# Kernel optimization log

Measured on AMD Instinct MI355X. Metric: run time of the kernel, lower is better.

Reference implementation:

```python
import jax, jax.numpy as jnp
import numpy as np

B, LP, NC, D, E = 8, 1000, 64, 128, 320  # batch, protein len, compound atoms, hid dim, esm dim


def _linear_params(key, din, dout):
    k1, k2 = jax.random.split(key)
    lim = 1.0 / np.sqrt(din)
    W = jax.random.uniform(k1, (din, dout), minval=-lim, maxval=lim, dtype=jnp.float32)
    b = jax.random.uniform(k2, (dout,), minval=-lim, maxval=lim, dtype=jnp.float32)
    return W, b


def setup_inputs() -> dict:
    key = jax.random.key(0)
    ks = jax.random.split(key, 14)
    inp = {
        "protein_embedding": jax.random.normal(ks[0], (B, LP, E), dtype=jnp.float32),
        "protein_feat_x": jax.random.normal(ks[1], (B, LP, D), dtype=jnp.float32),
        "compound_feats": jax.random.normal(ks[2], (B, NC, D), dtype=jnp.float32),
    }
    layers = [("emb", E, D), ("wq", D, D), ("wk", D, D), ("wv", D, D), ("wo", D, D),
              ("jp", D, D), ("jc", D, D),
              ("c1", D, 1024), ("c2", 1024, 1024), ("c3", 1024, 256), ("c4", 256, 1)]
    for i, (name, din, dout) in enumerate(layers):
        W, b = _linear_params(ks[3 + i], din, dout)
        inp[name + "_w"] = W
        inp[name + "_b"] = b
    return inp


def reference(protein_embedding, protein_feat_x, compound_feats,
              emb_w, emb_b, wq_w, wq_b, wk_w, wk_b, wv_w, wv_b, wo_w, wo_b,
              jp_w, jp_b, jc_w, jc_b,
              c1_w, c1_b, c2_w, c2_b, c3_w, c3_b, c4_w, c4_b):
    # protein sequence embedding -> hid dim
    pe = protein_embedding @ emb_w + emb_b                      # [B, LP, D]
    # single-head cross attention: query = seq embedding, key/value = graph feats
    Q = pe @ wq_w + wq_b
    K = protein_feat_x @ wk_w + wk_b
    V = protein_feat_x @ wv_w + wv_b
    scale = jnp.sqrt(jnp.asarray(D, pe.dtype))                  # n_heads=1 -> head_dim=D
    attn = jax.nn.softmax(jnp.einsum('bqd,bkd->bqk', Q, K) / scale, axis=-1)
    protein_feats = jnp.einsum('bqk,bkd->bqd', attn, V) @ wo_w + wo_b  # [B, LP, D]

    # sigmoid bilinear joint attention over (protein residue, compound atom) pairs
    P = jax.nn.relu(protein_feats) @ jp_w + jp_b                # [B, LP, D]
    C = jax.nn.relu(compound_feats) @ jc_w + jc_b               # [B, NC, D]
    A = jax.nn.sigmoid(jnp.einsum('bid,bkd->bik', P, C))        # [B, LP, NC]
    A = A / jnp.sum(A, axis=(1, 2), keepdims=True)

    # tanh outer product (the costly 4D bikj intermediate) then weighted reduction
    cp = jnp.tanh(protein_feats[:, :, None, :] * compound_feats[:, None, :, :])  # [B, LP, NC, D]
    cp_embedding = jnp.einsum('bikd,bik->bd', cp, A)            # [B, D]

    # classifier MLP (dropout is eval-mode identity)
    h = jax.nn.relu(cp_embedding @ c1_w + c1_b)
    h = jax.nn.relu(h @ c2_w + c2_b)
    h = jax.nn.relu(h @ c3_w + c3_b)
    return h @ c4_w + c4_b                                      # [B, 1]
```

## Files before the change

kernel.cpp:

```cpp
#include <hip/hip_runtime.h>
#include <hip/hip_bf16.h>
#include <math.h>

#define LP 1000
#define NCMP 64
#define NSPLIT 3

__device__ __forceinline__ float rcp_fast(float x) { return __builtin_amdgcn_rcpf(x); }

template<bool RELU_IN>
__device__ __forceinline__ void gemm_body(const float* X, const float* W, const float* __restrict__ bias,
                                          float* Y, int K, int rowbase)
{
    __shared__ __align__(16) float Ws[32][128];
    __shared__ __align__(16) float Xt[32][36];
    const int t  = threadIdx.x;
    const int r0 = (t >> 5) * 4;
    const int c0 = (t & 31) * 4;
    const int xr = t >> 3, xk = (t & 7) << 2;
    const int xrow = rowbase + xr;
    float4 xv = *(const float4*)(X + (long)xrow * K + xk);
    float4 wv[4];
    #pragma unroll
    for (int u = 0; u < 4; ++u) {
        int s = t + u * 256, r = s >> 5, cb = (s & 31) << 2;
        wv[u] = *(const float4*)(W + (long)r * 128 + cb);
    }
    float acc[4][4] = {};
    for (int k0 = 0; k0 < K; k0 += 32) {
        float4 xs = xv;
        if (RELU_IN) { xs.x = fmaxf(xs.x,0.f); xs.y = fmaxf(xs.y,0.f);
                       xs.z = fmaxf(xs.z,0.f); xs.w = fmaxf(xs.w,0.f); }
        Xt[xk+0][xr] = xs.x; Xt[xk+1][xr] = xs.y; Xt[xk+2][xr] = xs.z; Xt[xk+3][xr] = xs.w;
        #pragma unroll
        for (int u = 0; u < 4; ++u) {
            int s = t + u * 256, r = s >> 5, cb = (s & 31) << 2;
            *(float4*)&Ws[r][cb] = wv[u];
        }
        __syncthreads();
        if (k0 + 32 < K) {
            xv = *(const float4*)(X + (long)xrow * K + k0 + 32 + xk);
            #pragma unroll
            for (int u = 0; u < 4; ++u) {
                int s = t + u * 256, r = s >> 5, cb = (s & 31) << 2;
                wv[u] = *(const float4*)(W + (long)(k0 + 32 + r) * 128 + cb);
            }
        }
        #pragma unroll
        for (int kk = 0; kk < 32; ++kk) {
            float4 w4 = *(const float4*)&Ws[kk][c0];
            float4 x4 = *(const float4*)&Xt[kk][r0];
            acc[0][0] = fmaf(x4.x, w4.x, acc[0][0]); acc[0][1] = fmaf(x4.x, w4.y, acc[0][1]);
            acc[0][2] = fmaf(x4.x, w4.z, acc[0][2]); acc[0][3] = fmaf(x4.x, w4.w, acc[0][3]);
            acc[1][0] = fmaf(x4.y, w4.x, acc[1][0]); acc[1][1] = fmaf(x4.y, w4.y, acc[1][1]);
            acc[1][2] = fmaf(x4.y, w4.z, acc[1][2]); acc[1][3] = fmaf(x4.y, w4.w, acc[1][3]);
            acc[2][0] = fmaf(x4.z, w4.x, acc[2][0]); acc[2][1] = fmaf(x4.z, w4.y, acc[2][1]);
            acc[2][2] = fmaf(x4.z, w4.z, acc[2][2]); acc[2][3] = fmaf(x4.z, w4.w, acc[2][3]);
            acc[3][0] = fmaf(x4.w, w4.x, acc[3][0]); acc[3][1] = fmaf(x4.w, w4.y, acc[3][1]);
            acc[3][2] = fmaf(x4.w, w4.z, acc[3][2]); acc[3][3] = fmaf(x4.w, w4.w, acc[3][3]);
        }
        __syncthreads();
    }
    float4 bv = *(const float4*)(bias + c0);
    #pragma unroll
    for (int i = 0; i < 4; ++i) {
        int row = rowbase + r0 + i;
        float4 o;
        o.x = acc[i][0] + bv.x; o.y = acc[i][1] + bv.y;
        o.z = acc[i][2] + bv.z; o.w = acc[i][3] + bv.w;
        *(float4*)(Y + (long)row * 128 + c0) = o;
    }
}

__global__ __launch_bounds__(256) void pre0_k(const float* __restrict__ emb_w, const float* __restrict__ emb_b,
                                              const float* __restrict__ wq_w, const float* __restrict__ wq_b,
                                              const float* __restrict__ wv_w, const float* __restrict__ wv_b,
                                              const float* __restrict__ wo_w, const float* __restrict__ wo_b,
                                              const float* __restrict__ zeros,
                                              float* __restrict__ Wp, float* __restrict__ bp,
                                              float* __restrict__ Wvo, float* __restrict__ bvo)
{
    const int bid = blockIdx.x;
    if (bid < 10) { gemm_body<false>(emb_w, wq_w, zeros, Wp, 128, bid * 32); return; }
    if (bid >= 11 && bid < 15) { gemm_body<false>(wv_w, wo_w, zeros, Wvo, 128, (bid - 11) * 32); return; }
    int n = threadIdx.x;
    if (n < 128) {
        const float* vb = (bid == 10) ? emb_b : wv_b;
        const float* Wm = (bid == 10) ? wq_w  : wo_w;
        const float* ab = (bid == 10) ? wq_b  : wo_b;
        float a0 = 0.f, a1 = 0.f, a2 = 0.f, a3 = 0.f;
        for (int k = 0; k < 128; k += 4) {
            a0 = fmaf(vb[k+0], Wm[(k+0)*128 + n], a0);
            a1 = fmaf(vb[k+1], Wm[(k+1)*128 + n], a1);
            a2 = fmaf(vb[k+2], Wm[(k+2)*128 + n], a2);
            a3 = fmaf(vb[k+3], Wm[(k+3)*128 + n], a3);
        }
        float* dst = (bid == 10) ? bp : bvo;
        dst[n] = (a0 + a1) + (a2 + a3) + ab[n];
    }
}

__global__ __launch_bounds__(256) void qkv_k(const float* __restrict__ PE, const float* __restrict__ Wp,
                                             const float* __restrict__ bp, const float* __restrict__ PFX,
                                             const float* __restrict__ wk_w, const float* __restrict__ wk_b,
                                             const float* __restrict__ CF, const float* __restrict__ jc_w,
                                             const float* __restrict__ jc_b,
                                             float* __restrict__ Qo, float* __restrict__ Ko, float* __restrict__ Cj)
{
    if (blockIdx.x < 250)
        gemm_body<false>(PE, Wp, bp, Qo, 320, blockIdx.x * 32);
    else if (blockIdx.x < 500)
        gemm_body<false>(PFX, wk_w, wk_b, Ko, 128, (blockIdx.x - 250) * 32);
    else
        gemm_body<true>(CF, jc_w, jc_b, Cj, 128, (blockIdx.x - 500) * 32);
}

__global__ __launch_bounds__(256) void flash6_k(const float* __restrict__ Q, const float* __restrict__ Kg,
                                                const float* __restrict__ Vg, float* __restrict__ Opart,
                                                float* __restrict__ mpart, float* __restrict__ lpart)
{
    __shared__ __align__(16) float Qs[48][132];
    __shared__ __align__(16) float KVs[64][132];
    __shared__ __align__(16) float Ps[48][68];
    const int t  = threadIdx.x;
    const int tr = t >> 4;
    const int tc = t & 15;
    const int qt = blockIdx.x, sp = blockIdx.y, b = blockIdx.z;
    const int q0 = qt * 48;
    const int kt0 = (sp * 16) / NSPLIT;
    const int kt1 = ((sp + 1) * 16) / NSPLIT;
    const float SCALE = 0.08838834764831845f;
    const float L2E   = 1.4426950408889634f;

    #pragma unroll
    for (int u = 0; u < 6; ++u) {
        int s = t + u * 256, r = s >> 5, cb = (s & 31) << 2;
        float4 v = make_float4(0.f, 0.f, 0.f, 0.f);
        if (q0 + r < LP) v = *(const float4*)(Q + ((long)b * LP + q0 + r) * 128 + cb);
        *(float4*)&Qs[r][cb] = v;
    }
    float m_i[3] = { -3.0e38f, -3.0e38f, -3.0e38f };
    float l_i[3] = { 0.f, 0.f, 0.f };
    float Oa[3][8] = {};

    for (int kt = kt0; kt < kt1; ++kt) {
        const int key0 = kt * 64;
        __syncthreads();
        #pragma unroll
        for (int u = 0; u < 8; ++u) {
            int s = t + u * 256, r = s >> 5, cb = (s & 31) << 2;
            float4 v = make_float4(0.f, 0.f, 0.f, 0.f);
            if (key0 + r < LP) v = *(const float4*)(Kg + ((long)b * LP + key0 + r) * 128 + cb);
            *(float4*)&KVs[r][cb] = v;
        }
        __syncthreads();
        float sacc[3][4] = {};
        #pragma unroll 4
        for (int d4 = 0; d4 < 32; ++d4) {
            float4 q0v = *(const float4*)&Qs[3 * tr + 0][d4 << 2];
            float4 q1v = *(const float4*)&Qs[3 * tr + 1][d4 << 2];
            float4 q2v = *(const float4*)&Qs[3 * tr + 2][d4 << 2];
            #pragma unroll
            for (int j = 0; j < 4; ++j) {
                float4 kv = *(const float4*)&KVs[tc + (j << 4)][d4 << 2];
                sacc[0][j] += q0v.x*kv.x + q0v.y*kv.y + q0v.z*kv.z + q0v.w*kv.w;
                sacc[1][j] += q1v.x*kv.x + q1v.y*kv.y + q1v.z*kv.z + q1v.w*kv.w;
                sacc[2][j] += q2v.x*kv.x + q2v.y*kv.y + q2v.z*kv.z + q2v.w*kv.w;
            }
        }
        __syncthreads();
        float4 vreg[8];
        #pragma unroll
        for (int u = 0; u < 8; ++u) {
            int s = t + u * 256, r = s >> 5, cb = (s & 31) << 2;
            vreg[u] = make_float4(0.f, 0.f, 0.f, 0.f);
            if (key0 + r < LP) vreg[u] = *(const float4*)(Vg + ((long)b * LP + key0 + r) * 128 + cb);
        }
        #pragma unroll
        for (int j = 0; j < 4; ++j) {
            bool valid = (key0 + tc + (j << 4)) < LP;
            #pragma unroll
            for (int i = 0; i < 3; ++i) {
                float sv = sacc[i][j] * SCALE;
                sacc[i][j] = valid ? sv : -3.0e38f;
            }
        }
        #pragma unroll
        for (int i = 0; i < 3; ++i) {
            float tm = fmaxf(fmaxf(sacc[i][0], sacc[i][1]), fmaxf(sacc[i][2], sacc[i][3]));
            tm = fmaxf(tm, __shfl_xor(tm, 1));
            tm = fmaxf(tm, __shfl_xor(tm, 2));
            tm = fmaxf(tm, __shfl_xor(tm, 4));
            tm = fmaxf(tm, __shfl_xor(tm, 8));
            float mnew  = fmaxf(m_i[i], tm);
            float alpha = exp2f((m_i[i] - mnew) * L2E);
            float ps = 0.f;
            #pragma unroll
            for (int j = 0; j < 4; ++j) {
                float p = exp2f((sacc[i][j] - mnew) * L2E);
                Ps[3 * tr + i][tc + (j << 4)] = p;
                ps += p;
            }
            ps += __shfl_xor(ps, 1);
            ps += __shfl_xor(ps, 2);
            ps += __shfl_xor(ps, 4);
            ps += __shfl_xor(ps, 8);
            l_i[i] = l_i[i] * alpha + ps;
            m_i[i] = mnew;
            #pragma unroll
            for (int j = 0; j < 8; ++j) Oa[i][j] *= alpha;
        }
        #pragma unroll
        for (int u = 0; u < 8; ++u) {
            int s = t + u * 256, r = s >> 5, cb = (s & 31) << 2;
            *(float4*)&KVs[r][cb] = vreg[u];
        }
        __syncthreads();
        #pragma unroll 2
        for (int cg = 0; cg < 16; ++cg) {
            float4 pa = *(const float4*)&Ps[3 * tr + 0][cg << 2];
            float4 pb = *(const float4*)&Ps[3 * tr + 1][cg << 2];
            float4 pc = *(const float4*)&Ps[3 * tr + 2][cg << 2];
            #pragma unroll
            for (int e = 0; e < 4; ++e) {
                int c = (cg << 2) + e;
                float4 va = *(const float4*)&KVs[c][tc << 2];
                float4 vb = *(const float4*)&KVs[c][64 + (tc << 2)];
                float p0 = (e == 0) ? pa.x : (e == 1) ? pa.y : (e == 2) ? pa.z : pa.w;
                float p1 = (e == 0) ? pb.x : (e == 1) ? pb.y : (e == 2) ? pb.z : pb.w;
                float p2 = (e == 0) ? pc.x : (e == 1) ? pc.y : (e == 2) ? pc.z : pc.w;
                Oa[0][0] = fmaf(p0, va.x, Oa[0][0]); Oa[0][1] = fmaf(p0, va.y, Oa[0][1]);
                Oa[0][2] = fmaf(p0, va.z, Oa[0][2]); Oa[0][3] = fmaf(p0, va.w, Oa[0][3]);
                Oa[0][4] = fmaf(p0, vb.x, Oa[0][4]); Oa[0][5] = fmaf(p0, vb.y, Oa[0][5]);
                Oa[0][6] = fmaf(p0, vb.z, Oa[0][6]); Oa[0][7] = fmaf(p0, vb.w, Oa[0][7]);
                Oa[1][0] = fmaf(p1, va.x, Oa[1][0]); Oa[1][1] = fmaf(p1, va.y, Oa[1][1]);
                Oa[1][2] = fmaf(p1, va.z, Oa[1][2]); Oa[1][3] = fmaf(p1, va.w, Oa[1][3]);
                Oa[1][4] = fmaf(p1, vb.x, Oa[1][4]); Oa[1][5] = fmaf(p1, vb.y, Oa[1][5]);
                Oa[1][6] = fmaf(p1, vb.z, Oa[1][6]); Oa[1][7] = fmaf(p1, vb.w, Oa[1][7]);
                Oa[2][0] = fmaf(p2, va.x, Oa[2][0]); Oa[2][1] = fmaf(p2, va.y, Oa[2][1]);
                Oa[2][2] = fmaf(p2, va.z, Oa[2][2]); Oa[2][3] = fmaf(p2, va.w, Oa[2][3]);
                Oa[2][4] = fmaf(p2, vb.x, Oa[2][4]); Oa[2][5] = fmaf(p2, vb.y, Oa[2][5]);
                Oa[2][6] = fmaf(p2, vb.z, Oa[2][6]); Oa[2][7] = fmaf(p2, vb.w, Oa[2][7]);
            }
        }
    }
    #pragma unroll
    for (int i = 0; i < 3; ++i) {
        int row = q0 + 3 * tr + i;
        if (row < LP) {
            long base = ((long)sp * 1024000) + ((long)b * LP + row) * 128;
            *(float4*)(Opart + base + (tc << 2))      = make_float4(Oa[i][0], Oa[i][1], Oa[i][2], Oa[i][3]);
            *(float4*)(Opart + base + 64 + (tc << 2)) = make_float4(Oa[i][4], Oa[i][5], Oa[i][6], Oa[i][7]);
            if (tc == 0) {
                mpart[(long)sp * 8000 + b * LP + row] = m_i[i];
                lpart[(long)sp * 8000 + b * LP + row] = l_i[i];
            }
        }
    }
}

__global__ __launch_bounds__(256) void megatail_k(
    const float* __restrict__ Opart, const float* __restrict__ mp, const float* __restrict__ lp,
    const float* __restrict__ Wvo, const float* __restrict__ bvo,
    const float* __restrict__ jp_w, const float* __restrict__ jp_b,
    const float* __restrict__ Cj, const float* __restrict__ CF,
    float* __restrict__ Asum, float* __restrict__ cpe)
{
    __shared__ __align__(16) float WsA[32][132];
    __shared__ __align__(16) float Xt[32][20];
    __shared__ __align__(16) float AttS[16][132];
    __shared__ __align__(16) float Csh[64][132];
    __shared__ float Ash[16][64];
    __shared__ float red[256];
    const int t = threadIdx.x;
    const int p0 = blockIdx.x * 16;
    const int b  = blockIdx.y;
    const float L2E = 1.4426950408889634f;

    #pragma unroll
    for (int u = 0; u < 8; ++u) {
        int s = t + u * 256, r = s >> 5, cb = (s & 31) << 2;
        *(float4*)&Csh[r][cb] = *(const float4*)(Cj + ((long)b * NCMP + r) * 128 + cb);
    }

    const int r0 = (t >> 5) * 2, c0 = (t & 31) * 4;
    const int xr = t >> 3, xk = (t & 7) << 2;
    int prow = p0 + xr; if (prow > LP - 1) prow = LP - 1;
    const long g = (long)b * LP + prow;
    float wgt[NSPLIT]; float linv = 0.f;
    if (t < 128) {
        float mm = -3.0e38f;
        #pragma unroll
        for (int s = 0; s < NSPLIT; ++s) mm = fmaxf(mm, mp[g + (long)s * 8000]);
        float ls = 0.f;
        #pragma unroll
        for (int s = 0; s < NSPLIT; ++s) {
            wgt[s] = exp2f((mp[g + (long)s * 8000] - mm) * L2E);
            ls += wgt[s] * lp[g + (long)s * 8000];
        }
        linv = 1.0f / ls;
    }
    float4 xv = make_float4(0.f,0.f,0.f,0.f);
    float4 wv[4];
    if (t < 128) {
        float4 a = make_float4(0.f,0.f,0.f,0.f);
        #pragma unroll
        for (int s = 0; s < NSPLIT; ++s) {
            float4 p = *(const float4*)(Opart + (long)s * 1024000 + g * 128 + xk);
            a.x = fmaf(wgt[s], p.x, a.x); a.y = fmaf(wgt[s], p.y, a.y);
            a.z = fmaf(wgt[s], p.z, a.z); a.w = fmaf(wgt[s], p.w, a.w);
        }
        xv = make_float4(a.x * linv, a.y * linv, a.z * linv, a.w * linv);
    }
    #pragma unroll
    for (int u = 0; u < 4; ++u) {
        int s = t + u * 256, r = s >> 5, cb = (s & 31) << 2;
        wv[u] = *(const float4*)(Wvo + (long)r * 128 + cb);
    }
    float acc[2][4] = {};
    for (int k0 = 0; k0 < 128; k0 += 32) {
        if (t < 128) { Xt[xk+0][xr]=xv.x; Xt[xk+1][xr]=xv.y; Xt[xk+2][xr]=xv.z; Xt[xk+3][xr]=xv.w; }
        #pragma unroll
        for (int u = 0; u < 4; ++u) {
            int s = t + u * 256, r = s >> 5, cb = (s & 31) << 2;
            *(float4*)&WsA[r][cb] = wv[u];
        }
        __syncthreads();
        if (k0 + 32 < 128) {
            int kn = k0 + 32;
            if (t < 128) {
                float4 a = make_float4(0.f,0.f,0.f,0.f);
                #pragma unroll
                for (int s = 0; s < NSPLIT; ++s) {
                    float4 p = *(const float4*)(Opart + (long)s * 1024000 + g * 128 + kn + xk);
                    a.x = fmaf(wgt[s], p.x, a.x); a.y = fmaf(wgt[s], p.y, a.y);
                    a.z = fmaf(wgt[s], p.z, a.z); a.w = fmaf(wgt[s], p.w, a.w);
                }
                xv = make_float4(a.x * linv, a.y * linv, a.z * linv, a.w * linv);
            }
            #pragma unroll
            for (int u = 0; u < 4; ++u) {
                int s = t + u * 256, r = s >> 5, cb = (s & 31) << 2;
                wv[u] = *(const float4*)(Wvo + (long)(kn + r) * 128 + cb);
            }
        }
        #pragma unroll
        for (int kk = 0; kk < 32; ++kk) {
            float2 x2 = *(const float2*)&Xt[kk][r0];
            float4 w4 = *(const float4*)&WsA[kk][c0];
            acc[0][0]=fmaf(x2.x,w4.x,acc[0][0]); acc[0][1]=fmaf(x2.x,w4.y,acc[0][1]);
            acc[0][2]=fmaf(x2.x,w4.z,acc[0][2]); acc[0][3]=fmaf(x2.x,w4.w,acc[0][3]);
            acc[1][0]=fmaf(x2.y,w4.x,acc[1][0]); acc[1][1]=fmaf(x2.y,w4.y,acc[1][1]);
            acc[1][2]=fmaf(x2.y,w4.z,acc[1][2]); acc[1][3]=fmaf(x2.y,w4.w,acc[1][3]);
        }
        __syncthreads();
    }
    {
        float4 bv1 = *(const float4*)(bvo + c0);
        #pragma unroll
        for (int i = 0; i < 2; ++i)
            *(float4*)&AttS[r0 + i][c0] =
                make_float4(acc[i][0]+bv1.x, acc[i][1]+bv1.y, acc[i][2]+bv1.z, acc[i][3]+bv1.w);
    }
    float4 wv2[4];
    #pragma unroll
    for (int u = 0; u < 4; ++u) {
        int s = t + u * 256, r = s >> 5, cb = (s & 31) << 2;
        wv2[u] = *(const float4*)(jp_w + (long)r * 128 + cb);
    }
    float ac2[2][4] = {};
    for (int k0 = 0; k0 < 128; k0 += 32) {
        #pragma unroll
        for (int u = 0; u < 4; ++u) {
            int s = t + u * 256, r = s >> 5, cb = (s & 31) << 2;
            *(float4*)&WsA[r][cb] = wv2[u];
        }
        __syncthreads();
        if (k0 + 32 < 128) {
            #pragma unroll
            for (int u = 0; u < 4; ++u) {
                int s = t + u * 256, r = s >> 5, cb = (s & 31) << 2;
                wv2[u] = *(const float4*)(jp_w + (long)(k0 + 32 + r) * 128 + cb);
            }
        }
        #pragma unroll
        for (int kk = 0; kk < 32; ++kk) {
            float x0 = fmaxf(AttS[r0 + 0][k0 + kk], 0.f);
            float x1 = fmaxf(AttS[r0 + 1][k0 + kk], 0.f);
            float4 w4 = *(const float4*)&WsA[kk][c0];
            ac2[0][0]=fmaf(x0,w4.x,ac2[0][0]); ac2[0][1]=fmaf(x0,w4.y,ac2[0][1]);
            ac2[0][2]=fmaf(x0,w4.z,ac2[0][2]); ac2[0][3]=fmaf(x0,w4.w,ac2[0][3]);
            ac2[1][0]=fmaf(x1,w4.x,ac2[1][0]); ac2[1][1]=fmaf(x1,w4.y,ac2[1][1]);
            ac2[1][2]=fmaf(x1,w4.z,ac2[1][2]); ac2[1][3]=fmaf(x1,w4.w,ac2[1][3]);
        }
        __syncthreads();
    }
    float (*Psh)[132] = WsA;
    {
        float4 b2 = *(const float4*)(jp_b + c0);
        #pragma unroll
        for (int i = 0; i < 2; ++i)
            *(float4*)&Psh[r0 + i][c0] =
                make_float4(ac2[i][0]+b2.x, ac2[i][1]+b2.y, ac2[i][2]+b2.z, ac2[i][3]+b2.w);
    }
    __syncthreads();
    const int tr = t >> 4, tc = t & 15;
    float sacc[4] = {};
    #pragma unroll 4
    for (int d4 = 0; d4 < 32; ++d4) {
        float4 p4 = *(const float4*)&Psh[tr][d4 << 2];
        #pragma unroll
        for (int j = 0; j < 4; ++j) {
            float4 cv = *(const float4*)&Csh[tc + (j << 4)][d4 << 2];
            sacc[j] += p4.x*cv.x + p4.y*cv.y + p4.z*cv.z + p4.w*cv.w;
        }
    }
    float lsum = 0.f;
    {
        int gi = p0 + tr;
        #pragma unroll
        for (int j = 0; j < 4; ++j) {
            float sg = rcp_fast(1.f + exp2f(-sacc[j] * L2E));
            if (gi < LP) { Ash[tr][tc + (j << 4)] = sg; lsum += sg; }
        }
    }
    red[t] = lsum;
    __syncthreads();
    for (int off = 128; off > 0; off >>= 1) {
        if (t < off) red[t] += red[t + off];
        __syncthreads();
    }
    if (t == 0) atomicAdd(Asum + b, red[0]);
    __syncthreads();
    #pragma unroll
    for (int u = 0; u < 8; ++u) {
        int s = t + u * 256, r = s >> 5, cb = (s & 31) << 2;
        *(float4*)&Csh[r][cb] = *(const float4*)(CF + ((long)b * NCMP + r) * 128 + cb);
    }
    __syncthreads();
    const float TWO_L2E = 2.8853900817779268f;
    const int d  = t & 127;
    const int kh = t >> 7;
    const int iiN = (LP - p0 < 16) ? (LP - p0) : 16;
    float accD = 0.f;
    for (int ii = 0; ii < iiN; ++ii) {
        float ptl = AttS[ii][d] * TWO_L2E;
        #pragma unroll
        for (int kk = 0; kk < 32; ++kk) {
            int k = (kh << 5) + kk;
            float e  = exp2f(ptl * Csh[k][d]);
            float th = 1.f - 2.f * rcp_fast(e + 1.f);
            accD = fmaf(th, Ash[ii][k], accD);
        }
    }
    red[t] = accD;
    __syncthreads();
    if (t < 128) atomicAdd(cpe + (long)b * 128 + t, red[t] + red[t + 128]);
}

__global__ __launch_bounds__(256) void c12_k(const float* __restrict__ cpe, const float* __restrict__ Asum,
                                             const float* __restrict__ c1_w, const float* __restrict__ c1_b,
                                             const float* __restrict__ c2_w, float* __restrict__ part)
{
    __shared__ float sc[8][128];
    __shared__ float ins[8][16];
    const int t = threadIdx.x, ks = blockIdx.x, k0 = ks * 16;
    #pragma unroll
    for (int u = 0; u < 4; ++u) {
        int idx = t + u * 256;
        sc[idx >> 7][idx & 127] = cpe[idx] * rcp_fast(Asum[idx >> 7]);
    }
    __syncthreads();
    if (t < 128) {
        int b = t >> 4, kk = t & 15;
        int n1 = k0 + kk;
        float a0 = 0.f, a1 = 0.f, a2 = 0.f, a3 = 0.f;
        #pragma unroll 8
        for (int j = 0; j < 128; j += 4) {
            a0 = fmaf(sc[b][j+0], c1_w[(long)(j+0)*1024 + n1], a0);
            a1 = fmaf(sc[b][j+1], c1_w[(long)(j+1)*1024 + n1], a1);
            a2 = fmaf(sc[b][j+2], c1_w[(long)(j+2)*1024 + n1], a2);
            a3 = fmaf(sc[b][j+3], c1_w[(long)(j+3)*1024 + n1], a3);
        }
        ins[b][kk] = fmaxf((a0 + a1) + (a2 + a3) + c1_b[n1], 0.f);
    }
    __syncthreads();
    const int n = (t & 63) * 4 + (t >> 6) * 256;
    float4 acc[8] = {};
    #pragma unroll
    for (int kk = 0; kk < 16; ++kk) {
        float4 w4 = *(const float4*)(c2_w + (long)(k0 + kk) * 1024 + n);
        #pragma unroll
        for (int b = 0; b < 8; ++b) {
            float s = ins[b][kk];
            acc[b].x = fmaf(s, w4.x, acc[b].x); acc[b].y = fmaf(s, w4.y, acc[b].y);
            acc[b].z = fmaf(s, w4.z, acc[b].z); acc[b].w = fmaf(s, w4.w, acc[b].w);
        }
    }
    #pragma unroll
    for (int b = 0; b < 8; ++b)
        *(float4*)(part + ((long)(ks * 8 + b)) * 1024 + n) = acc[b];
}

__global__ __launch_bounds__(256) void c3m_k(const float* __restrict__ part2, const float* __restrict__ c2_b,
                                             const float* __restrict__ c3_w, const float* __restrict__ c3_b,
                                             const float* __restrict__ c4_w, const float* __restrict__ c4_b,
                                             float* __restrict__ out)
{
    __shared__ float Hs[1024];
    __shared__ float red[256];
    const int t = threadIdx.x, b = blockIdx.x;
    float4 acc4 = make_float4(0.f,0.f,0.f,0.f);
    #pragma unroll 4
    for (int ks = 0; ks < 64; ++ks) {
        float4 p = *(const float4*)(part2 + ((long)(ks * 8 + b)) * 1024 + t * 4);
        acc4.x += p.x; acc4.y += p.y; acc4.z += p.z; acc4.w += p.w;
    }
    {
        float4 bb = *(const float4*)(c2_b + t * 4);
        Hs[t*4+0] = fmaxf(acc4.x + bb.x, 0.f);
        Hs[t*4+1] = fmaxf(acc4.y + bb.y, 0.f);
        Hs[t*4+2] = fmaxf(acc4.z + bb.z, 0.f);
        Hs[t*4+3] = fmaxf(acc4.w + bb.w, 0.f);
    }
    __syncthreads();
    float a0 = 0.f, a1 = 0.f, a2 = 0.f, a3 = 0.f;
    #pragma unroll 8
    for (int k = 0; k < 1024; k += 4) {
        a0 = fmaf(Hs[k+0], c3_w[(long)(k+0)*256 + t], a0);
        a1 = fmaf(Hs[k+1], c3_w[(long)(k+1)*256 + t], a1);
        a2 = fmaf(Hs[k+2], c3_w[(long)(k+2)*256 + t], a2);
        a3 = fmaf(Hs[k+3], c3_w[(long)(k+3)*256 + t], a3);
    }
    float h3v = fmaxf((a0 + a1) + (a2 + a3) + c3_b[t], 0.f);
    red[t] = h3v * c4_w[t];
    __syncthreads();
    for (int off = 128; off > 0; off >>= 1) {
        if (t < off) red[t] += red[t + off];
        __syncthreads();
    }
    if (t == 0) out[b] = red[0] + c4_b[0];
}

extern "C" void kernel_launch(void* const* d_in, const int* in_sizes, int n_in,
                              void* d_out, int out_size, void* d_ws, size_t ws_size,
                              hipStream_t stream)
{
    const float* PE   = (const float*)d_in[0];
    const float* PFX  = (const float*)d_in[1];
    const float* CF   = (const float*)d_in[2];
    const float* emb_w = (const float*)d_in[3];  const float* emb_b = (const float*)d_in[4];
    const float* wq_w  = (const float*)d_in[5];  const float* wq_b  = (const float*)d_in[6];
    const float* wk_w  = (const float*)d_in[7];  const float* wk_b  = (const float*)d_in[8];
    const float* wv_w  = (const float*)d_in[9];  const float* wv_b  = (const float*)d_in[10];
    const float* wo_w  = (const float*)d_in[11]; const float* wo_b  = (const float*)d_in[12];
    const float* jp_w  = (const float*)d_in[13]; const float* jp_b  = (const float*)d_in[14];
    const float* jc_w  = (const float*)d_in[15]; const float* jc_b  = (const float*)d_in[16];
    const float* c1_w  = (const float*)d_in[17]; const float* c1_b  = (const float*)d_in[18];
    const float* c2_w  = (const float*)d_in[19]; const float* c2_b  = (const float*)d_in[20];
    const float* c3_w  = (const float*)d_in[21]; const float* c3_b  = (const float*)d_in[22];
    const float* c4_w  = (const float*)d_in[23]; const float* c4_b  = (const float*)d_in[24];

    float* ws     = (float*)d_ws;
    float* bufQ   = ws;
    float* bufK   = bufQ   + 1024000;
    float* bufC   = bufK   + 1024000;
    float* Opart  = bufC   + 65536;
    float* mpart  = Opart  + 3072000;
    float* lpart  = mpart  + 24000;
    float* Asum   = lpart  + 24000;
    float* cpe    = Asum   + 8;
    float* zeros  = cpe    + 1024;
    float* bprime = zeros  + 128;
    float* bufWp  = bprime + 128;
    float* bufWvo = bufWp  + 40960;
    float* bufbvo = bufWvo + 16384;
    float* part2  = bufQ;

    hipMemsetAsync(Asum, 0, (8 + 1024 + 128) * sizeof(float), stream);

    pre0_k<<<16, 256, 0, stream>>>(emb_w, emb_b, wq_w, wq_b, wv_w, wv_b, wo_w, wo_b,
                                   zeros, bufWp, bprime, bufWvo, bufbvo);
    qkv_k<<<516, 256, 0, stream>>>(PE, bufWp, bprime, PFX, wk_w, wk_b, CF, jc_w, jc_b,
                                   bufQ, bufK, bufC);
    flash6_k<<<dim3(21, NSPLIT, 8), 256, 0, stream>>>(bufQ, bufK, PFX, Opart, mpart, lpart);
    megatail_k<<<dim3(63, 8), 256, 0, stream>>>(Opart, mpart, lpart, bufWvo, bufbvo,
                                                jp_w, jp_b, bufC, CF, Asum, cpe);
    c12_k<<<64, 256, 0, stream>>>(cpe, Asum, c1_w, c1_b, c2_w, part2);
    c3m_k<<<8, 256, 0, stream>>>(part2, c2_b, c3_w, c3_b, c4_w, c4_b, (float*)d_out);
}
```

Before: 336.5 us.

## Fold memset into pre0, restructure tanh-reduction loop, widen c12 split

The separate hipMemsetAsync is removed, and spare threads of block 10 in pre0_k now zero Asum and cpe, with the zero-bias buffer replaced by a NO_BIAS template flag. In megatail_k, the ReLU'd attention rows for the jp GEMM are read as float4. The tanh outer-product loop is reordered to iterate compounds outermost, with protein values held in registers and a transposed sigmoid matrix read as float4. c12_k is split across 128 blocks of 8 columns instead of 64 of 16, which doubles the partial-sum rows that c3m_k must reduce. Together these aim to cut a launch, raise parallelism in the classifier, and reduce LDS traffic in the hot tanh loop.

```diff
diff --git a/kernel.cpp b/kernel.cpp
--- a/kernel.cpp
+++ b/kernel.cpp
@@ -8,7 +8,7 @@
 
 __device__ __forceinline__ float rcp_fast(float x) { return __builtin_amdgcn_rcpf(x); }
 
-template<bool RELU_IN>
+template<bool RELU_IN, bool NO_BIAS>
 __device__ __forceinline__ void gemm_body(const float* X, const float* W, const float* __restrict__ bias,
                                           float* Y, int K, int rowbase)
 {
@@ -61,7 +61,7 @@
         }
         __syncthreads();
     }
-    float4 bv = *(const float4*)(bias + c0);
+    float4 bv = NO_BIAS ? make_float4(0.f,0.f,0.f,0.f) : *(const float4*)(bias + c0);
     #pragma unroll
     for (int i = 0; i < 4; ++i) {
         int row = rowbase + r0 + i;
@@ -76,27 +76,31 @@
                                               const float* __restrict__ wq_w, const float* __restrict__ wq_b,
                                               const float* __restrict__ wv_w, const float* __restrict__ wv_b,
                                               const float* __restrict__ wo_w, const float* __restrict__ wo_b,
-                                              const float* __restrict__ zeros,
                                               float* __restrict__ Wp, float* __restrict__ bp,
-                                              float* __restrict__ Wvo, float* __restrict__ bvo)
+                                              float* __restrict__ Wvo, float* __restrict__ bvo,
+                                              float* __restrict__ zbase)
 {
     const int bid = blockIdx.x;
-    if (bid < 10) { gemm_body<false>(emb_w, wq_w, zeros, Wp, 128, bid * 32); return; }
-    if (bid >= 11 && bid < 15) { gemm_body<false>(wv_w, wo_w, zeros, Wvo, 128, (bid - 11) * 32); return; }
-    int n = threadIdx.x;
-    if (n < 128) {
+    if (bid < 10) { gemm_body<false,true>(emb_w, wq_w, nullptr, Wp, 128, bid * 32); return; }
+    if (bid >= 11 && bid < 15) { gemm_body<false,true>(wv_w, wo_w, nullptr, Wvo, 128, (bid - 11) * 32); return; }
+    int t = threadIdx.x;
+    if (bid == 10 && t >= 128) {
+        for (int i = t - 128; i < 1032; i += 128) zbase[i] = 0.f;
+        return;
+    }
+    if (t < 128) {
         const float* vb = (bid == 10) ? emb_b : wv_b;
         const float* Wm = (bid == 10) ? wq_w  : wo_w;
         const float* ab = (bid == 10) ? wq_b  : wo_b;
         float a0 = 0.f, a1 = 0.f, a2 = 0.f, a3 = 0.f;
         for (int k = 0; k < 128; k += 4) {
-            a0 = fmaf(vb[k+0], Wm[(k+0)*128 + n], a0);
-            a1 = fmaf(vb[k+1], Wm[(k+1)*128 + n], a1);
-            a2 = fmaf(vb[k+2], Wm[(k+2)*128 + n], a2);
-            a3 = fmaf(vb[k+3], Wm[(k+3)*128 + n], a3);
+            a0 = fmaf(vb[k+0], Wm[(k+0)*128 + t], a0);
+            a1 = fmaf(vb[k+1], Wm[(k+1)*128 + t], a1);
+            a2 = fmaf(vb[k+2], Wm[(k+2)*128 + t], a2);
+            a3 = fmaf(vb[k+3], Wm[(k+3)*128 + t], a3);
         }
         float* dst = (bid == 10) ? bp : bvo;
-        dst[n] = (a0 + a1) + (a2 + a3) + ab[n];
+        dst[t] = (a0 + a1) + (a2 + a3) + ab[t];
     }
 }
 
@@ -108,11 +112,11 @@
                                              float* __restrict__ Qo, float* __restrict__ Ko, float* __restrict__ Cj)
 {
     if (blockIdx.x < 250)
-        gemm_body<false>(PE, Wp, bp, Qo, 320, blockIdx.x * 32);
+        gemm_body<false,false>(PE, Wp, bp, Qo, 320, blockIdx.x * 32);
     else if (blockIdx.x < 500)
-        gemm_body<false>(PFX, wk_w, wk_b, Ko, 128, (blockIdx.x - 250) * 32);
+        gemm_body<false,false>(PFX, wk_w, wk_b, Ko, 128, (blockIdx.x - 250) * 32);
     else
-        gemm_body<true>(CF, jc_w, jc_b, Cj, 128, (blockIdx.x - 500) * 32);
+        gemm_body<true,false>(CF, jc_w, jc_b, Cj, 128, (blockIdx.x - 500) * 32);
 }
 
 __global__ __launch_bounds__(256) void flash6_k(const float* __restrict__ Q, const float* __restrict__ Kg,
@@ -270,7 +274,8 @@
     __shared__ __align__(16) float Xt[32][20];
     __shared__ __align__(16) float AttS[16][132];
     __shared__ __align__(16) float Csh[64][132];
-    __shared__ float Ash[16][64];
+    __shared__ __align__(16) float Ash[16][64];
+    __shared__ __align__(16) float AshT[64][20];
     __shared__ float red[256];
     const int t = threadIdx.x;
     const int p0 = blockIdx.x * 16;
@@ -384,14 +389,19 @@
             }
         }
         #pragma unroll
-        for (int kk = 0; kk < 32; ++kk) {
-            float x0 = fmaxf(AttS[r0 + 0][k0 + kk], 0.f);
-            float x1 = fmaxf(AttS[r0 + 1][k0 + kk], 0.f);
-            float4 w4 = *(const float4*)&WsA[kk][c0];
-            ac2[0][0]=fmaf(x0,w4.x,ac2[0][0]); ac2[0][1]=fmaf(x0,w4.y,ac2[0][1]);
-            ac2[0][2]=fmaf(x0,w4.z,ac2[0][2]); ac2[0][3]=fmaf(x0,w4.w,ac2[0][3]);
-            ac2[1][0]=fmaf(x1,w4.x,ac2[1][0]); ac2[1][1]=fmaf(x1,w4.y,ac2[1][1]);
-            ac2[1][2]=fmaf(x1,w4.z,ac2[1][2]); ac2[1][3]=fmaf(x1,w4.w,ac2[1][3]);
+        for (int kq = 0; kq < 8; ++kq) {
+            float4 xa = *(const float4*)&AttS[r0 + 0][k0 + (kq << 2)];
+            float4 xb = *(const float4*)&AttS[r0 + 1][k0 + (kq << 2)];
+            #pragma unroll
+            for (int e = 0; e < 4; ++e) {
+                float x0 = fmaxf((e==0)?xa.x:(e==1)?xa.y:(e==2)?xa.z:xa.w, 0.f);
+                float x1 = fmaxf((e==0)?xb.x:(e==1)?xb.y:(e==2)?xb.z:xb.w, 0.f);
+                float4 w4 = *(const float4*)&WsA[(kq << 2) + e][c0];
+                ac2[0][0]=fmaf(x0,w4.x,ac2[0][0]); ac2[0][1]=fmaf(x0,w4.y,ac2[0][1]);
+                ac2[0][2]=fmaf(x0,w4.z,ac2[0][2]); ac2[0][3]=fmaf(x0,w4.w,ac2[0][3]);
+                ac2[1][0]=fmaf(x1,w4.x,ac2[1][0]); ac2[1][1]=fmaf(x1,w4.y,ac2[1][1]);
+                ac2[1][2]=fmaf(x1,w4.z,ac2[1][2]); ac2[1][3]=fmaf(x1,w4.w,ac2[1][3]);
+            }
         }
         __syncthreads();
     }
@@ -421,7 +431,11 @@
         #pragma unroll
         for (int j = 0; j < 4; ++j) {
             float sg = rcp_fast(1.f + exp2f(-sacc[j] * L2E));
-            if (gi < LP) { Ash[tr][tc + (j << 4)] = sg; lsum += sg; }
+            if (gi < LP) {
+                Ash[tr][tc + (j << 4)]  = sg;
+                AshT[tc + (j << 4)][tr] = sg;
+                lsum += sg;
+            }
         }
     }
     red[t] = lsum;
@@ -442,15 +456,23 @@
     const int d  = t & 127;
     const int kh = t >> 7;
     const int iiN = (LP - p0 < 16) ? (LP - p0) : 16;
+    float areg[16];
+    #pragma unroll
+    for (int ii = 0; ii < 16; ++ii) areg[ii] = AttS[ii][d] * TWO_L2E;
     float accD = 0.f;
-    for (int ii = 0; ii < iiN; ++ii) {
-        float ptl = AttS[ii][d] * TWO_L2E;
-        #pragma unroll
-        for (int kk = 0; kk < 32; ++kk) {
-            int k = (kh << 5) + kk;
-            float e  = exp2f(ptl * Csh[k][d]);
-            float th = 1.f - 2.f * rcp_fast(e + 1.f);
-            accD = fmaf(th, Ash[ii][k], accD);
+    for (int kk = 0; kk < 32; ++kk) {
+        const int k = (kh << 5) + kk;
+        const float cv = Csh[k][d];
+        for (int iq = 0; iq < iiN; iq += 4) {
+            float4 a4 = *(const float4*)&AshT[k][iq];
+            float e0 = exp2f(areg[iq+0] * cv);
+            float e1 = exp2f(areg[iq+1] * cv);
+            float e2 = exp2f(areg[iq+2] * cv);
+            float e3 = exp2f(areg[iq+3] * cv);
+            accD = fmaf(1.f - 2.f * rcp_fast(e0 + 1.f), a4.x, accD);
+            accD = fmaf(1.f - 2.f * rcp_fast(e1 + 1.f), a4.y, accD);
+            accD = fmaf(1.f - 2.f * rcp_fast(e2 + 1.f), a4.z, accD);
+            accD = fmaf(1.f - 2.f * rcp_fast(e3 + 1.f), a4.w, accD);
         }
     }
     red[t] = accD;
@@ -463,16 +485,16 @@
                                              const float* __restrict__ c2_w, float* __restrict__ part)
 {
     __shared__ float sc[8][128];
-    __shared__ float ins[8][16];
-    const int t = threadIdx.x, ks = blockIdx.x, k0 = ks * 16;
+    __shared__ float ins[8][8];
+    const int t = threadIdx.x, ks = blockIdx.x, k0 = ks * 8;
     #pragma unroll
     for (int u = 0; u < 4; ++u) {
         int idx = t + u * 256;
         sc[idx >> 7][idx & 127] = cpe[idx] * rcp_fast(Asum[idx >> 7]);
     }
     __syncthreads();
-    if (t < 128) {
-        int b = t >> 4, kk = t & 15;
+    if (t < 64) {
+        int b = t >> 3, kk = t & 7;
         int n1 = k0 + kk;
         float a0 = 0.f, a1 = 0.f, a2 = 0.f, a3 = 0.f;
         #pragma unroll 8
@@ -488,7 +510,7 @@
     const int n = (t & 63) * 4 + (t >> 6) * 256;
     float4 acc[8] = {};
     #pragma unroll
-    for (int kk = 0; kk < 16; ++kk) {
+    for (int kk = 0; kk < 8; ++kk) {
         float4 w4 = *(const float4*)(c2_w + (long)(k0 + kk) * 1024 + n);
         #pragma unroll
         for (int b = 0; b < 8; ++b) {
@@ -512,7 +534,7 @@
     const int t = threadIdx.x, b = blockIdx.x;
     float4 acc4 = make_float4(0.f,0.f,0.f,0.f);
     #pragma unroll 4
-    for (int ks = 0; ks < 64; ++ks) {
+    for (int ks = 0; ks < 128; ++ks) {
         float4 p = *(const float4*)(part2 + ((long)(ks * 8 + b)) * 1024 + t * 4);
         acc4.x += p.x; acc4.y += p.y; acc4.z += p.z; acc4.w += p.w;
     }
@@ -570,22 +592,19 @@
     float* lpart  = mpart  + 24000;
     float* Asum   = lpart  + 24000;
     float* cpe    = Asum   + 8;
-    float* zeros  = cpe    + 1024;
-    float* bprime = zeros  + 128;
+    float* bprime = cpe    + 1024;
     float* bufWp  = bprime + 128;
     float* bufWvo = bufWp  + 40960;
     float* bufbvo = bufWvo + 16384;
     float* part2  = bufQ;
 
-    hipMemsetAsync(Asum, 0, (8 + 1024 + 128) * sizeof(float), stream);
-
     pre0_k<<<16, 256, 0, stream>>>(emb_w, emb_b, wq_w, wq_b, wv_w, wv_b, wo_w, wo_b,
-                                   zeros, bufWp, bprime, bufWvo, bufbvo);
+                                   bufWp, bprime, bufWvo, bufbvo, Asum);
     qkv_k<<<516, 256, 0, stream>>>(PE, bufWp, bprime, PFX, wk_w, wk_b, CF, jc_w, jc_b,
                                    bufQ, bufK, bufC);
     flash6_k<<<dim3(21, NSPLIT, 8), 256, 0, stream>>>(bufQ, bufK, PFX, Opart, mpart, lpart);
     megatail_k<<<dim3(63, 8), 256, 0, stream>>>(Opart, mpart, lpart, bufWvo, bufbvo,
                                                 jp_w, jp_b, bufC, CF, Asum, cpe);
-    c12_k<<<64, 256, 0, stream>>>(cpe, Asum, c1_w, c1_b, c2_w, part2);
+    c12_k<<<128, 256, 0, stream>>>(cpe, Asum, c1_w, c1_b, c2_w, part2);
     c3m_k<<<8, 256, 0, stream>>>(part2, c2_b, c3_w, c3_b, c4_w, c4_b, (float*)d_out);
 }
```

New measurement: 337.9 us. About the same (+0.4%).
